# Kernel optimization log

Measured on AMD Instinct MI355X. Metric: run time of the kernel, lower is better.

Reference implementation:

```python
import jax, jax.numpy as jnp
import numpy as np

B, L, E = 2, 2048, 1024
H = 16
DH = E // H  # head dim for qk and v (dim_qk=dim_v=embed_dim)
HID = 4 * E  # fcn_dim_factor * dim_v
SCALE = DH ** 0.5


def setup_inputs() -> dict:
    key = jax.random.key(0)
    ks = jax.random.split(key, 12)
    s = lambda fan_in: 1.0 / np.sqrt(fan_in)
    return {
        "x": jax.random.uniform(ks[0], (B, L), jnp.float32),
        "z": jax.random.normal(ks[1], (B, L, E), jnp.float32),
        "Wq": jax.random.normal(ks[2], (E, E), jnp.float32) * s(E),
        "bq": jnp.zeros((E,), jnp.float32),
        "Wk": jax.random.normal(ks[3], (E, E), jnp.float32) * s(E),
        "bk": jnp.zeros((E,), jnp.float32),
        "Wv": jax.random.normal(ks[4], (E, E), jnp.float32) * s(E),
        "bv": jnp.zeros((E,), jnp.float32),
        "W1": jax.random.normal(ks[5], (E, HID), jnp.float32) * s(E),
        "b1": jnp.zeros((HID,), jnp.float32),
        "W2": jax.random.normal(ks[6], (HID, 1), jnp.float32) * s(HID),
        "b2": jnp.zeros((1,), jnp.float32),
    }


def reference(x, z, Wq, bq, Wk, bk, Wv, bv, W1, b1, W2, b2):
    # Projections -> (B, H, L, DH)
    def heads(t):
        return t.reshape(B, L, H, DH).transpose(0, 2, 1, 3)

    Q = heads(z @ Wq + bq)
    K = heads(z @ Wk + bk)
    V = heads(z @ Wv + bv)

    # Scores (B, H, L, L)
    S = jnp.einsum("bhid,bhjd->bhij", Q, K) / SCALE

    # Weighted softmax along query axis (dim=-2), weighted by population x
    w = x[:, None, :, None]  # (B, 1, L, 1), broadcasts over queries i
    m = jnp.max(S, axis=-2, keepdims=True)
    e = w * jnp.exp(S - m)
    A = e / jnp.sum(e, axis=-2, keepdims=True)

    # V scaled by population weight, then AV
    V_scaled = w * V
    O = jnp.einsum("bhij,bhjd->bhid", A, V_scaled)  # (B, H, L, DH)
    O = O.transpose(0, 2, 1, 3).reshape(B, L, H * DH)

    # FFN: Linear -> GELU (exact) -> Linear(->1) -> squeeze
    y = jax.nn.gelu(O @ W1 + b1, approximate=False)
    y = (y @ W2 + b2).squeeze(-1)  # (B, L)
    return y
```

## Files before the change

### kernel.cpp

```cpp
#include <hip/hip_runtime.h>
#include <hip/hip_bf16.h>
#include <math.h>

#define B_    2
#define L_    2048
#define E_    1024
#define H_    16
#define DH_   64
#define HID_  4096
#define NROW_ (B_*L_)
#define BH_   (B_*H_)

typedef __attribute__((ext_vector_type(8)))  short    short8v;
typedef _Float16 half8v __attribute__((ext_vector_type(8)));
typedef __attribute__((ext_vector_type(16))) float    f32x16;

#define MFMA32(A, Bv, C) __builtin_amdgcn_mfma_f32_32x32x16_bf16((A), (Bv), (C), 0, 0, 0)
#define MFMAH(A, Bv, C)  __builtin_amdgcn_mfma_f32_32x32x16_f16((A), (Bv), (C), 0, 0, 0)

__device__ __forceinline__ unsigned short f2bf(float f) {
    union { float f; unsigned u; } v; v.f = f;
    unsigned r = v.u + 0x7FFF + ((v.u >> 16) & 1);
    return (unsigned short)(r >> 16);
}
__device__ __forceinline__ float bf2f(unsigned short u) {
    union { unsigned u; float f; } v; v.u = ((unsigned)u) << 16;
    return v.f;
}

__device__ __forceinline__ void gl_lds16(const void* g, void* l) {
    __builtin_amdgcn_global_load_lds(
        (const __attribute__((address_space(1))) unsigned int*)g,
        (__attribute__((address_space(3))) unsigned int*)l, 16, 0, 0);
}

__device__ __forceinline__ float erf_fast(float v) {
    float a = fabsf(v);
    float t = __builtin_amdgcn_rcpf(1.0f + 0.3275911f * a);
    float p = t * (0.254829592f + t * (-0.284496736f + t * (1.421413741f +
              t * (-1.453152027f + t * 1.061405429f))));
    float r = 1.0f - p * __expf(-a * a);
    return copysignf(r, v);
}

__global__ __launch_bounds__(256) void zh_prep(
    const float* __restrict__ z, _Float16* __restrict__ zh)
{
    const size_t i = ((size_t)blockIdx.x * 256 + threadIdx.x) * 8;
    float4 a = *(const float4*)&z[i];
    float4 b = *(const float4*)&z[i + 4];
    union { _Float16 h[8]; half8v v; } o;
    o.h[0] = (_Float16)a.x; o.h[1] = (_Float16)a.y;
    o.h[2] = (_Float16)a.z; o.h[3] = (_Float16)a.w;
    o.h[4] = (_Float16)b.x; o.h[5] = (_Float16)b.y;
    o.h[6] = (_Float16)b.z; o.h[7] = (_Float16)b.w;
    *(half8v*)&zh[i] = o.v;
}

__global__ __launch_bounds__(256) void wprep3(
    const float* __restrict__ Wq, const float* __restrict__ Wk,
    const float* __restrict__ Wv,
    _Float16* __restrict__ Tq, _Float16* __restrict__ Tk,
    _Float16* __restrict__ Tv)
{
    const float* src = (blockIdx.z == 0) ? Wq : (blockIdx.z == 1) ? Wk : Wv;
    _Float16*    dst = (blockIdx.z == 0) ? Tq : (blockIdx.z == 1) ? Tk : Tv;
    __shared__ float tile[64][65];
    const int t  = threadIdx.x;
    const int r0 = blockIdx.y * 64, c0 = blockIdx.x * 64;
    #pragma unroll
    for (int u = 0; u < 4; ++u) {
        int f = t + 256 * u, row = f >> 4, c4 = (f & 15) << 2;
        *(float4*)&tile[row][c4] = *(const float4*)&src[(size_t)(r0 + row) * E_ + c0 + c4];
    }
    __syncthreads();
    #pragma unroll
    for (int u = 0; u < 4; ++u) {
        int f = t + 256 * u, c = f >> 4, r4 = (f & 15) << 2;
        union { _Float16 h[4]; uint2 u2; } pk;
        pk.h[0] = (_Float16)tile[r4 + 0][c];
        pk.h[1] = (_Float16)tile[r4 + 1][c];
        pk.h[2] = (_Float16)tile[r4 + 2][c];
        pk.h[3] = (_Float16)tile[r4 + 3][c];
        *(uint2*)&dst[(size_t)(c0 + c) * E_ + r0 + r4] = pk.u2;
    }
}

__global__ __launch_bounds__(256) void w1prep(
    const float* __restrict__ W1, _Float16* __restrict__ W1t)
{
    __shared__ float tile[64][65];
    const int t  = threadIdx.x;
    const int r0 = blockIdx.y * 64, c0 = blockIdx.x * 64;
    #pragma unroll
    for (int u = 0; u < 4; ++u) {
        int f = t + 256 * u, row = f >> 4, c4 = (f & 15) << 2;
        *(float4*)&tile[row][c4] = *(const float4*)&W1[(size_t)(r0 + row) * HID_ + c0 + c4];
    }
    __syncthreads();
    #pragma unroll
    for (int u = 0; u < 4; ++u) {
        int f = t + 256 * u, c = f >> 4, r4 = (f & 15) << 2;
        union { _Float16 h[4]; uint2 u2; } pk;
        pk.h[0] = (_Float16)tile[r4 + 0][c];
        pk.h[1] = (_Float16)tile[r4 + 1][c];
        pk.h[2] = (_Float16)tile[r4 + 2][c];
        pk.h[3] = (_Float16)tile[r4 + 3][c];
        *(uint2*)&W1t[(size_t)(c0 + c) * E_ + r0 + r4] = pk.u2;
    }
}

__global__ __launch_bounds__(512) void qkv_mfma(
    const _Float16* __restrict__ zh,
    const _Float16* __restrict__ Tq, const _Float16* __restrict__ Tk,
    const _Float16* __restrict__ Tv,
    const float* __restrict__ bq, const float* __restrict__ bk,
    const float* __restrict__ bv,
    unsigned short* __restrict__ Qo, unsigned short* __restrict__ Ko,
    unsigned short* __restrict__ Vo)
{
    const int which = blockIdx.z;
    const _Float16* Wt = (which == 0) ? Tq : (which == 1) ? Tk : Tv;
    const float*  bias = (which == 0) ? bq : (which == 1) ? bk : bv;
    unsigned short* out = (which == 0) ? Qo : (which == 1) ? Ko : Vo;

    __shared__ _Float16 Ah[256 * 64];
    __shared__ _Float16 Bs[256 * 64];

    const int t    = threadIdx.x;
    const int lane = t & 63;
    const int w    = t >> 6;
    const int l31  = lane & 31;
    const int hq   = lane >> 5;
    const int wm   = w >> 2, wn = w & 3;
    const int m0   = blockIdx.x * 256;
    const int n0   = blockIdx.y * 256;

    f32x16 acc[4][2] = {};

    for (int kc = 0; kc < 16; ++kc) {
        __syncthreads();
        #pragma unroll
        for (int u = 0; u < 4; ++u) {
            int ch  = w * 4 + u;
            int row = ch * 8 + (lane >> 3), s = lane & 7;
            gl_lds16(&zh[(size_t)(m0 + row) * E_ + kc * 64 + ((s ^ (row & 7)) << 3)], &Ah[ch * 512]);
            gl_lds16(&Wt[(size_t)(n0 + row) * E_ + kc * 64 + ((s ^ (row & 7)) << 3)], &Bs[ch * 512]);
        }
        __syncthreads();

        #pragma unroll
        for (int ks = 0; ks < 4; ++ks) {
            half8v fb[2];
            #pragma unroll
            for (int nb = 0; nb < 2; ++nb) {
                int br = wn * 64 + nb * 32 + l31;
                fb[nb] = *(const half8v*)&Bs[br * 64 + (((ks * 2 + hq) ^ (br & 7)) << 3)];
            }
            #pragma unroll
            for (int mb = 0; mb < 4; ++mb) {
                int ar = wm * 128 + mb * 32 + l31;
                half8v fa = *(const half8v*)&Ah[ar * 64 + (((ks * 2 + hq) ^ (ar & 7)) << 3)];
                acc[mb][0] = MFMAH(fa, fb[0], acc[mb][0]);
                acc[mb][1] = MFMAH(fa, fb[1], acc[mb][1]);
            }
        }
    }

    #pragma unroll
    for (int nb = 0; nb < 2; ++nb) {
        int n  = n0 + wn * 64 + nb * 32 + l31;
        int h  = n >> 6, dh = n & 63;
        float bb = bias[n];
        #pragma unroll
        for (int mb = 0; mb < 4; ++mb) {
            #pragma unroll
            for (int r = 0; r < 16; ++r) {
                int m  = m0 + wm * 128 + mb * 32 + (r & 3) + 8 * (r >> 2) + 4 * hq;
                int b  = m >> 11, i = m & (L_ - 1);
                out[((size_t)(b * H_ + h) * L_ + i) * DH_ + dh] = f2bf(acc[mb][nb][r] + bb);
            }
        }
    }
}

__global__ __launch_bounds__(256) void col_stats_mfma(
    const unsigned short* __restrict__ Qb, const unsigned short* __restrict__ Kb,
    const float* __restrict__ x, float* __restrict__ Do)
{
    __shared__ unsigned short Qlds[128 * 64];
    __shared__ float xlds[L_];

    const int t    = threadIdx.x;
    const int lane = t & 63;
    const int wv   = t >> 6;
    const int l31  = lane & 31;
    const int hq   = lane >> 5;
    const int bh   = blockIdx.y;
    const int b    = bh >> 4;
    const int j0   = blockIdx.x * 128 + wv * 32;

    #pragma unroll
    for (int u = 0; u < 2; ++u) {
        int f = t + 256 * u;
        *(float4*)&xlds[f * 4] = *(const float4*)&x[(size_t)b * L_ + f * 4];
    }

    short8v kf[4];
    {
        const unsigned short* kp = Kb + ((size_t)bh * L_ + j0 + l31) * DH_ + hq * 8;
        #pragma unroll
        for (int c = 0; c < 4; ++c) kf[c] = *(const short8v*)(kp + c * 16);
    }

    float d[16];
    #pragma unroll
    for (int r = 0; r < 16; ++r) d[r] = 0.f;

    for (int ich = 0; ich < L_ / 128; ++ich) {
        __syncthreads();
        #pragma unroll
        for (int u = 0; u < 4; ++u) {
            int ch  = wv * 4 + u;
            int row = ch * 8 + (lane >> 3), s = lane & 7;
            gl_lds16(&Qb[((size_t)bh * L_ + ich * 128 + row) * DH_ + ((s ^ (row & 7)) << 3)],
                     &Qlds[ch * 512]);
        }
        __syncthreads();

        #pragma unroll
        for (int cc = 0; cc < 4; ++cc) {
            f32x16 acc = {};
            #pragma unroll
            for (int c = 0; c < 4; ++c) {
                int qr = cc * 32 + l31;
                short8v qv = *(const short8v*)&Qlds[qr * 64 + (((c * 2 + hq) ^ (qr & 7)) << 3)];
                acc = MFMA32(kf[c], qv, acc);
            }
            float xi = xlds[ich * 128 + cc * 32 + l31];
            #pragma unroll
            for (int r = 0; r < 16; ++r)
                d[r] += xi * __expf(acc[r] * 0.125f);
        }
    }

    #pragma unroll
    for (int r = 0; r < 16; ++r) {
        #pragma unroll
        for (int off = 16; off > 0; off >>= 1)
            d[r] += __shfl_xor(d[r], off);
    }
    if (l31 == 0) {
        #pragma unroll
        for (int r = 0; r < 16; ++r)
            Do[(size_t)bh * L_ + j0 + 4 * hq + (r & 3) + 8 * (r >> 2)] = d[r];
    }
}

__global__ __launch_bounds__(256) void vt_prep(
    const unsigned short* __restrict__ Vb, const float* __restrict__ x,
    const float* __restrict__ Do, unsigned short* __restrict__ Vt)
{
    const int bh = blockIdx.y;
    const int b  = bh >> 4;
    const int j  = blockIdx.x * 256 + threadIdx.x;
    const float s = x[(size_t)b * L_ + j] / Do[(size_t)bh * L_ + j];
    const unsigned short* vp = Vb + ((size_t)bh * L_ + j) * DH_;
    #pragma unroll
    for (int c = 0; c < 16; ++c) {
        ushort4 v = *(const ushort4*)&vp[c * 4];
        Vt[((size_t)bh * DH_ + c * 4 + 0) * L_ + j] = f2bf(bf2f(v.x) * s);
        Vt[((size_t)bh * DH_ + c * 4 + 1) * L_ + j] = f2bf(bf2f(v.y) * s);
        Vt[((size_t)bh * DH_ + c * 4 + 2) * L_ + j] = f2bf(bf2f(v.z) * s);
        Vt[((size_t)bh * DH_ + c * 4 + 3) * L_ + j] = f2bf(bf2f(v.w) * s);
    }
}

__global__ __launch_bounds__(256) void attn_out_mfma(
    const unsigned short* __restrict__ Qb, const unsigned short* __restrict__ Kb,
    const unsigned short* __restrict__ Vt, const float* __restrict__ x,
    _Float16* __restrict__ Of)
{
    __shared__ unsigned short Klds[64 * 64];
    __shared__ unsigned short Vlds[64 * 64];
    __shared__ unsigned short Plds[4 * 32 * 64];

    const int t    = threadIdx.x;
    const int lane = t & 63;
    const int wv   = t >> 6;
    const int l31  = lane & 31;
    const int hq   = lane >> 5;
    const int bh   = blockIdx.y;
    const int b    = bh >> 4, hh = bh & 15;
    const int iw   = blockIdx.x * 128 + wv * 32;

    short8v qf[4];
    {
        const unsigned short* qp = Qb + ((size_t)bh * L_ + iw + l31) * DH_ + hq * 8;
        #pragma unroll
        for (int c = 0; c < 4; ++c) qf[c] = *(const short8v*)(qp + c * 16);
    }

    f32x16 accO0 = {}, accO1 = {};
    char* Pw = (char*)(Plds + wv * 2048);

    for (int jt = 0; jt < L_ / 64; ++jt) {
        int j0 = jt * 64;
        __syncthreads();
        #pragma unroll
        for (int u = 0; u < 2; ++u) {
            int ch  = wv * 2 + u;
            int row = ch * 8 + (lane >> 3), s = lane & 7;
            gl_lds16(&Kb[((size_t)bh * L_ + j0 + row) * DH_ + ((s ^ (row & 7)) << 3)], &Klds[ch * 512]);
            gl_lds16(&Vt[((size_t)bh * DH_ + row) * L_ + j0 + ((s ^ (row & 7)) << 3)], &Vlds[ch * 512]);
        }
        __syncthreads();

        #pragma unroll
        for (int js = 0; js < 2; ++js) {
            f32x16 as = {};
            #pragma unroll
            for (int c = 0; c < 4; ++c) {
                int krow = js * 32 + l31;
                short8v kfr = *(const short8v*)&Klds[krow * 64 + (((c * 2 + hq) ^ (krow & 7)) << 3)];
                as = MFMA32(kfr, qf[c], as);
            }
            #pragma unroll
            for (int q = 0; q < 4; ++q) {
                float p0 = __expf(as[4 * q + 0] * 0.125f);
                float p1 = __expf(as[4 * q + 1] * 0.125f);
                float p2 = __expf(as[4 * q + 2] * 0.125f);
                float p3 = __expf(as[4 * q + 3] * 0.125f);
                uint2 pk;
                pk.x = (unsigned)f2bf(p0) | ((unsigned)f2bf(p1) << 16);
                pk.y = (unsigned)f2bf(p2) | ((unsigned)f2bf(p3) << 16);
                int jb = js * 64 + 8 * hq + 16 * q;
                *(uint2*)(Pw + l31 * 128 + (jb ^ ((l31 & 7) << 4))) = pk;
            }
        }

        short8v pf[4];
        #pragma unroll
        for (int c = 0; c < 4; ++c)
            pf[c] = *(const short8v*)(Pw + l31 * 128 + (((c * 16 + hq * 8) * 2) ^ ((l31 & 7) << 4)));
        #pragma unroll
        for (int c = 0; c < 4; ++c) {
            int r0 = l31, r1 = 32 + l31;
            short8v vf0 = *(const short8v*)&Vlds[r0 * 64 + (((c * 2 + hq) ^ (r0 & 7)) << 3)];
            short8v vf1 = *(const short8v*)&Vlds[r1 * 64 + (((c * 2 + hq) ^ (r1 & 7)) << 3)];
            accO0 = MFMA32(pf[c], vf0, accO0);
            accO1 = MFMA32(pf[c], vf1, accO1);
        }
    }

    #pragma unroll
    for (int q = 0; q < 4; ++q) {
        float4 xq = *(const float4*)&x[(size_t)b * L_ + iw + 4 * hq + 8 * q];
        const float xs[4] = { xq.x, xq.y, xq.z, xq.w };
        #pragma unroll
        for (int k = 0; k < 4; ++k) {
            int r    = q * 4 + k;
            int irow = iw + 4 * hq + 8 * q + k;
            size_t base = ((size_t)b * L_ + irow) * E_ + hh * DH_;
            Of[base + l31]      = (_Float16)(accO0[r] * xs[k]);
            Of[base + 32 + l31] = (_Float16)(accO1[r] * xs[k]);
        }
    }
}

__global__ __launch_bounds__(256) void y_init(float* __restrict__ y, const float* __restrict__ b2)
{
    y[blockIdx.x * 256 + threadIdx.x] = b2[0];
}

__global__ __launch_bounds__(512) void mlp_mfma(
    const _Float16* __restrict__ Of, const _Float16* __restrict__ W1t,
    const float* __restrict__ b1, const float* __restrict__ W2,
    float* __restrict__ y)
{
    __shared__ _Float16 Oh[256 * 64];
    __shared__ _Float16 Wh[256 * 64];

    const int t    = threadIdx.x;
    const int lane = t & 63;
    const int w    = t >> 6;
    const int l31  = lane & 31;
    const int hq   = lane >> 5;
    const int wm   = w >> 2, wn = w & 3;
    const int m0   = blockIdx.x * 256;
    const int n0   = blockIdx.y * 256;

    f32x16 acc[4][2] = {};

    for (int kc = 0; kc < 16; ++kc) {
        __syncthreads();
        #pragma unroll
        for (int u = 0; u < 4; ++u) {
            int ch  = w * 4 + u;
            int row = ch * 8 + (lane >> 3), s = lane & 7;
            gl_lds16(&Of[(size_t)(m0 + row) * E_ + kc * 64 + ((s ^ (row & 7)) << 3)], &Oh[ch * 512]);
            gl_lds16(&W1t[(size_t)(n0 + row) * E_ + kc * 64 + ((s ^ (row & 7)) << 3)], &Wh[ch * 512]);
        }
        __syncthreads();

        #pragma unroll
        for (int ks = 0; ks < 4; ++ks) {
            half8v fb[2];
            #pragma unroll
            for (int nb = 0; nb < 2; ++nb) {
                int br = wn * 64 + nb * 32 + l31;
                fb[nb] = *(const half8v*)&Wh[br * 64 + (((ks * 2 + hq) ^ (br & 7)) << 3)];
            }
            #pragma unroll
            for (int mb = 0; mb < 4; ++mb) {
                int ar = wm * 128 + mb * 32 + l31;
                half8v fa = *(const half8v*)&Oh[ar * 64 + (((ks * 2 + hq) ^ (ar & 7)) << 3)];
                acc[mb][0] = MFMAH(fa, fb[0], acc[mb][0]);
                acc[mb][1] = MFMAH(fa, fb[1], acc[mb][1]);
            }
        }
    }

    const int hid0 = n0 + wn * 64 + l31;
    const float bb0 = b1[hid0],      w20 = W2[hid0];
    const float bb1 = b1[hid0 + 32], w21 = W2[hid0 + 32];
    #pragma unroll
    for (int mb = 0; mb < 4; ++mb) {
        #pragma unroll
        for (int r = 0; r < 16; ++r) {
            float h0 = acc[mb][0][r] + bb0;
            float h1 = acc[mb][1][r] + bb1;
            float s  = 0.5f * h0 * (1.0f + erf_fast(h0 * 0.70710678f)) * w20
                     + 0.5f * h1 * (1.0f + erf_fast(h1 * 0.70710678f)) * w21;
            #pragma unroll
            for (int off = 16; off > 0; off >>= 1) s += __shfl_xor(s, off);
            if (l31 == 0) {
                int m = m0 + wm * 128 + mb * 32 + (r & 3) + 8 * (r >> 2) + 4 * hq;
                atomicAdd(&y[m], s);
            }
        }
    }
}

extern "C" void kernel_launch(void* const* d_in, const int* in_sizes, int n_in,
                              void* d_out, int out_size, void* d_ws, size_t ws_size,
                              hipStream_t stream)
{
    const float* x  = (const float*)d_in[0];
    const float* z  = (const float*)d_in[1];
    const float* Wq = (const float*)d_in[2];
    const float* bq = (const float*)d_in[3];
    const float* Wk = (const float*)d_in[4];
    const float* bk = (const float*)d_in[5];
    const float* Wv = (const float*)d_in[6];
    const float* bv = (const float*)d_in[7];
    const float* W1 = (const float*)d_in[8];
    const float* b1 = (const float*)d_in[9];
    const float* W2 = (const float*)d_in[10];
    const float* b2 = (const float*)d_in[11];
    float* y = (float*)d_out;

    const size_t NQ = (size_t)BH_ * L_ * DH_;
    unsigned short* p = (unsigned short*)d_ws;
    unsigned short* Qb  = p;  p += NQ;
    unsigned short* Kb  = p;  p += NQ;
    unsigned short* Vb  = p;  p += NQ;
    unsigned short* Vt  = p;  p += NQ;
    _Float16* zh  = (_Float16*)p;  p += (size_t)NROW_ * E_;
    _Float16* Tq  = (_Float16*)p;  p += (size_t)E_ * E_;
    _Float16* Tk  = (_Float16*)p;  p += (size_t)E_ * E_;
    _Float16* Tv  = (_Float16*)p;  p += (size_t)E_ * E_;
    _Float16* W1t = (_Float16*)p;  p += (size_t)HID_ * E_;
    _Float16* Ofp = (_Float16*)p;  p += (size_t)NROW_ * E_;
    float* Dw = (float*)p;

    zh_prep<<<dim3((NROW_ * E_) / (256 * 8)), 256, 0, stream>>>(z, zh);
    wprep3 <<<dim3(E_ / 64, E_ / 64, 3), 256, 0, stream>>>(Wq, Wk, Wv, Tq, Tk, Tv);
    w1prep <<<dim3(HID_ / 64, E_ / 64), 256, 0, stream>>>(W1, W1t);

    qkv_mfma<<<dim3(NROW_ / 256, E_ / 256, 3), 512, 0, stream>>>(
        zh, Tq, Tk, Tv, bq, bk, bv, Qb, Kb, Vb);

    col_stats_mfma<<<dim3(L_ / 128, BH_), 256, 0, stream>>>(Qb, Kb, x, Dw);

    vt_prep<<<dim3(L_ / 256, BH_), 256, 0, stream>>>(Vb, x, Dw, Vt);

    attn_out_mfma<<<dim3(L_ / 128, BH_), 256, 0, stream>>>(Qb, Kb, Vt, x, Ofp);

    y_init<<<dim3(NROW_ / 256), 256, 0, stream>>>(y, b2);

    mlp_mfma<<<dim3(NROW_ / 256, HID_ / 256), 512, 0, stream>>>(
        Ofp, W1t, b1, W2, y);
}
```

Baseline: 231.8 us.

## Double-buffer LDS tiles in GEMM and attention kernels to overlap loads with MFMA

Adds ping-pong LDS buffers to qkv_mfma, col_stats_mfma, attn_out_mfma and mlp_mfma. The next k-chunk is issued with global-to-LDS loads before the current chunk's MFMAs run, and each iteration ends with one barrier. The goal is to hide global load latency behind compute. In exchange, LDS use doubles: the GEMM kernels go to 128KB per block, which can cut occupancy to one block per CU. It also depends on the async LDS loads being complete by the time the single barrier is reached.

```diff
diff --git a/kernel.cpp b/kernel.cpp
--- a/kernel.cpp
+++ b/kernel.cpp
@@ -124,8 +124,8 @@
     const float*  bias = (which == 0) ? bq : (which == 1) ? bk : bv;
     unsigned short* out = (which == 0) ? Qo : (which == 1) ? Ko : Vo;
 
-    __shared__ _Float16 Ah[256 * 64];
-    __shared__ _Float16 Bs[256 * 64];
+    __shared__ _Float16 Ah[2][256 * 64];
+    __shared__ _Float16 Bs[2][256 * 64];
 
     const int t    = threadIdx.x;
     const int lane = t & 63;
@@ -136,18 +136,30 @@
     const int m0   = blockIdx.x * 256;
     const int n0   = blockIdx.y * 256;
 
+    const int srow0 = (lane >> 3);
+    const int ssl   = lane & 7;
+
     f32x16 acc[4][2] = {};
 
+#define QKV_STAGE(bb, kc)                                                          \
+    {                                                                              \
+        _Pragma("unroll")                                                          \
+        for (int u = 0; u < 4; ++u) {                                              \
+            int ch  = w * 4 + u;                                                   \
+            int row = ch * 8 + srow0;                                              \
+            gl_lds16(&zh[(size_t)(m0 + row) * E_ + (kc) * 64 + ((ssl ^ (row & 7)) << 3)], \
+                     &Ah[bb][ch * 512]);                                           \
+            gl_lds16(&Wt[(size_t)(n0 + row) * E_ + (kc) * 64 + ((ssl ^ (row & 7)) << 3)], \
+                     &Bs[bb][ch * 512]);                                           \
+        }                                                                          \
+    }
+
+    QKV_STAGE(0, 0);
+    __syncthreads();
+    int cur = 0;
+
     for (int kc = 0; kc < 16; ++kc) {
-        __syncthreads();
-        #pragma unroll
-        for (int u = 0; u < 4; ++u) {
-            int ch  = w * 4 + u;
-            int row = ch * 8 + (lane >> 3), s = lane & 7;
-            gl_lds16(&zh[(size_t)(m0 + row) * E_ + kc * 64 + ((s ^ (row & 7)) << 3)], &Ah[ch * 512]);
-            gl_lds16(&Wt[(size_t)(n0 + row) * E_ + kc * 64 + ((s ^ (row & 7)) << 3)], &Bs[ch * 512]);
-        }
-        __syncthreads();
+        if (kc < 15) QKV_STAGE(cur ^ 1, kc + 1);
 
         #pragma unroll
         for (int ks = 0; ks < 4; ++ks) {
@@ -155,16 +167,18 @@
             #pragma unroll
             for (int nb = 0; nb < 2; ++nb) {
                 int br = wn * 64 + nb * 32 + l31;
-                fb[nb] = *(const half8v*)&Bs[br * 64 + (((ks * 2 + hq) ^ (br & 7)) << 3)];
+                fb[nb] = *(const half8v*)&Bs[cur][br * 64 + (((ks * 2 + hq) ^ (br & 7)) << 3)];
             }
             #pragma unroll
             for (int mb = 0; mb < 4; ++mb) {
                 int ar = wm * 128 + mb * 32 + l31;
-                half8v fa = *(const half8v*)&Ah[ar * 64 + (((ks * 2 + hq) ^ (ar & 7)) << 3)];
+                half8v fa = *(const half8v*)&Ah[cur][ar * 64 + (((ks * 2 + hq) ^ (ar & 7)) << 3)];
                 acc[mb][0] = MFMAH(fa, fb[0], acc[mb][0]);
                 acc[mb][1] = MFMAH(fa, fb[1], acc[mb][1]);
             }
         }
+        __syncthreads();
+        cur ^= 1;
     }
 
     #pragma unroll
@@ -182,13 +196,14 @@
             }
         }
     }
+#undef QKV_STAGE
 }
 
 __global__ __launch_bounds__(256) void col_stats_mfma(
     const unsigned short* __restrict__ Qb, const unsigned short* __restrict__ Kb,
     const float* __restrict__ x, float* __restrict__ Do)
 {
-    __shared__ unsigned short Qlds[128 * 64];
+    __shared__ unsigned short Qlds[2][128 * 64];
     __shared__ float xlds[L_];
 
     const int t    = threadIdx.x;
@@ -200,6 +215,9 @@
     const int b    = bh >> 4;
     const int j0   = blockIdx.x * 128 + wv * 32;
 
+    const int srow0 = (lane >> 3);
+    const int ssl   = lane & 7;
+
     #pragma unroll
     for (int u = 0; u < 2; ++u) {
         int f = t + 256 * u;
@@ -217,16 +235,23 @@
     #pragma unroll
     for (int r = 0; r < 16; ++r) d[r] = 0.f;
 
+#define CS_STAGE(bb, ich)                                                           \
+    {                                                                               \
+        _Pragma("unroll")                                                           \
+        for (int u = 0; u < 4; ++u) {                                               \
+            int ch  = wv * 4 + u;                                                   \
+            int row = ch * 8 + srow0;                                               \
+            gl_lds16(&Qb[((size_t)bh * L_ + (ich) * 128 + row) * DH_ + ((ssl ^ (row & 7)) << 3)], \
+                     &Qlds[bb][ch * 512]);                                          \
+        }                                                                           \
+    }
+
+    CS_STAGE(0, 0);
+    __syncthreads();
+    int cur = 0;
+
     for (int ich = 0; ich < L_ / 128; ++ich) {
-        __syncthreads();
-        #pragma unroll
-        for (int u = 0; u < 4; ++u) {
-            int ch  = wv * 4 + u;
-            int row = ch * 8 + (lane >> 3), s = lane & 7;
-            gl_lds16(&Qb[((size_t)bh * L_ + ich * 128 + row) * DH_ + ((s ^ (row & 7)) << 3)],
-                     &Qlds[ch * 512]);
-        }
-        __syncthreads();
+        if (ich < L_ / 128 - 1) CS_STAGE(cur ^ 1, ich + 1);
 
         #pragma unroll
         for (int cc = 0; cc < 4; ++cc) {
@@ -234,7 +259,7 @@
             #pragma unroll
             for (int c = 0; c < 4; ++c) {
                 int qr = cc * 32 + l31;
-                short8v qv = *(const short8v*)&Qlds[qr * 64 + (((c * 2 + hq) ^ (qr & 7)) << 3)];
+                short8v qv = *(const short8v*)&Qlds[cur][qr * 64 + (((c * 2 + hq) ^ (qr & 7)) << 3)];
                 acc = MFMA32(kf[c], qv, acc);
             }
             float xi = xlds[ich * 128 + cc * 32 + l31];
@@ -242,6 +267,8 @@
             for (int r = 0; r < 16; ++r)
                 d[r] += xi * __expf(acc[r] * 0.125f);
         }
+        __syncthreads();
+        cur ^= 1;
     }
 
     #pragma unroll
@@ -255,6 +282,7 @@
         for (int r = 0; r < 16; ++r)
             Do[(size_t)bh * L_ + j0 + 4 * hq + (r & 3) + 8 * (r >> 2)] = d[r];
     }
+#undef CS_STAGE
 }
 
 __global__ __launch_bounds__(256) void vt_prep(
@@ -281,8 +309,8 @@
     const unsigned short* __restrict__ Vt, const float* __restrict__ x,
     _Float16* __restrict__ Of)
 {
-    __shared__ unsigned short Klds[64 * 64];
-    __shared__ unsigned short Vlds[64 * 64];
+    __shared__ unsigned short Klds[2][64 * 64];
+    __shared__ unsigned short Vlds[2][64 * 64];
     __shared__ unsigned short Plds[4 * 32 * 64];
 
     const int t    = threadIdx.x;
@@ -294,6 +322,9 @@
     const int b    = bh >> 4, hh = bh & 15;
     const int iw   = blockIdx.x * 128 + wv * 32;
 
+    const int srow0 = (lane >> 3);
+    const int ssl   = lane & 7;
+
     short8v qf[4];
     {
         const unsigned short* qp = Qb + ((size_t)bh * L_ + iw + l31) * DH_ + hq * 8;
@@ -304,17 +335,25 @@
     f32x16 accO0 = {}, accO1 = {};
     char* Pw = (char*)(Plds + wv * 2048);
 
+#define AO_STAGE(bb, jt)                                                            \
+    {                                                                               \
+        _Pragma("unroll")                                                           \
+        for (int u = 0; u < 2; ++u) {                                               \
+            int ch  = wv * 2 + u;                                                   \
+            int row = ch * 8 + srow0;                                               \
+            gl_lds16(&Kb[((size_t)bh * L_ + (jt) * 64 + row) * DH_ + ((ssl ^ (row & 7)) << 3)], \
+                     &Klds[bb][ch * 512]);                                          \
+            gl_lds16(&Vt[((size_t)bh * DH_ + row) * L_ + (jt) * 64 + ((ssl ^ (row & 7)) << 3)], \
+                     &Vlds[bb][ch * 512]);                                          \
+        }                                                                           \
+    }
+
+    AO_STAGE(0, 0);
+    __syncthreads();
+    int cur = 0;
+
     for (int jt = 0; jt < L_ / 64; ++jt) {
-        int j0 = jt * 64;
-        __syncthreads();
-        #pragma unroll
-        for (int u = 0; u < 2; ++u) {
-            int ch  = wv * 2 + u;
-            int row = ch * 8 + (lane >> 3), s = lane & 7;
-            gl_lds16(&Kb[((size_t)bh * L_ + j0 + row) * DH_ + ((s ^ (row & 7)) << 3)], &Klds[ch * 512]);
-            gl_lds16(&Vt[((size_t)bh * DH_ + row) * L_ + j0 + ((s ^ (row & 7)) << 3)], &Vlds[ch * 512]);
-        }
-        __syncthreads();
+        if (jt < L_ / 64 - 1) AO_STAGE(cur ^ 1, jt + 1);
 
         #pragma unroll
         for (int js = 0; js < 2; ++js) {
@@ -322,7 +361,7 @@
             #pragma unroll
             for (int c = 0; c < 4; ++c) {
                 int krow = js * 32 + l31;
-                short8v kfr = *(const short8v*)&Klds[krow * 64 + (((c * 2 + hq) ^ (krow & 7)) << 3)];
+                short8v kfr = *(const short8v*)&Klds[cur][krow * 64 + (((c * 2 + hq) ^ (krow & 7)) << 3)];
                 as = MFMA32(kfr, qf[c], as);
             }
             #pragma unroll
@@ -346,11 +385,13 @@
         #pragma unroll
         for (int c = 0; c < 4; ++c) {
             int r0 = l31, r1 = 32 + l31;
-            short8v vf0 = *(const short8v*)&Vlds[r0 * 64 + (((c * 2 + hq) ^ (r0 & 7)) << 3)];
-            short8v vf1 = *(const short8v*)&Vlds[r1 * 64 + (((c * 2 + hq) ^ (r1 & 7)) << 3)];
+            short8v vf0 = *(const short8v*)&Vlds[cur][r0 * 64 + (((c * 2 + hq) ^ (r0 & 7)) << 3)];
+            short8v vf1 = *(const short8v*)&Vlds[cur][r1 * 64 + (((c * 2 + hq) ^ (r1 & 7)) << 3)];
             accO0 = MFMA32(pf[c], vf0, accO0);
             accO1 = MFMA32(pf[c], vf1, accO1);
         }
+        __syncthreads();
+        cur ^= 1;
     }
 
     #pragma unroll
@@ -366,6 +407,7 @@
             Of[base + 32 + l31] = (_Float16)(accO1[r] * xs[k]);
         }
     }
+#undef AO_STAGE
 }
 
 __global__ __launch_bounds__(256) void y_init(float* __restrict__ y, const float* __restrict__ b2)
@@ -378,8 +420,8 @@
     const float* __restrict__ b1, const float* __restrict__ W2,
     float* __restrict__ y)
 {
-    __shared__ _Float16 Oh[256 * 64];
-    __shared__ _Float16 Wh[256 * 64];
+    __shared__ _Float16 Oh[2][256 * 64];
+    __shared__ _Float16 Wh[2][256 * 64];
 
     const int t    = threadIdx.x;
     const int lane = t & 63;
@@ -390,18 +432,30 @@
     const int m0   = blockIdx.x * 256;
     const int n0   = blockIdx.y * 256;
 
+    const int srow0 = (lane >> 3);
+    const int ssl   = lane & 7;
+
     f32x16 acc[4][2] = {};
 
+#define MLP_STAGE(bb, kc)                                                          \
+    {                                                                              \
+        _Pragma("unroll")                                                          \
+        for (int u = 0; u < 4; ++u) {                                              \
+            int ch  = w * 4 + u;                                                   \
+            int row = ch * 8 + srow0;                                              \
+            gl_lds16(&Of[(size_t)(m0 + row) * E_ + (kc) * 64 + ((ssl ^ (row & 7)) << 3)], \
+                     &Oh[bb][ch * 512]);                                           \
+            gl_lds16(&W1t[(size_t)(n0 + row) * E_ + (kc) * 64 + ((ssl ^ (row & 7)) << 3)], \
+                     &Wh[bb][ch * 512]);                                           \
+        }                                                                          \
+    }
+
+    MLP_STAGE(0, 0);
+    __syncthreads();
+    int cur = 0;
+
     for (int kc = 0; kc < 16; ++kc) {
-        __syncthreads();
-        #pragma unroll
-        for (int u = 0; u < 4; ++u) {
-            int ch  = w * 4 + u;
-            int row = ch * 8 + (lane >> 3), s = lane & 7;
-            gl_lds16(&Of[(size_t)(m0 + row) * E_ + kc * 64 + ((s ^ (row & 7)) << 3)], &Oh[ch * 512]);
-            gl_lds16(&W1t[(size_t)(n0 + row) * E_ + kc * 64 + ((s ^ (row & 7)) << 3)], &Wh[ch * 512]);
-        }
-        __syncthreads();
+        if (kc < 15) MLP_STAGE(cur ^ 1, kc + 1);
 
         #pragma unroll
         for (int ks = 0; ks < 4; ++ks) {
@@ -409,16 +463,18 @@
             #pragma unroll
             for (int nb = 0; nb < 2; ++nb) {
                 int br = wn * 64 + nb * 32 + l31;
-                fb[nb] = *(const half8v*)&Wh[br * 64 + (((ks * 2 + hq) ^ (br & 7)) << 3)];
+                fb[nb] = *(const half8v*)&Wh[cur][br * 64 + (((ks * 2 + hq) ^ (br & 7)) << 3)];
             }
             #pragma unroll
             for (int mb = 0; mb < 4; ++mb) {
                 int ar = wm * 128 + mb * 32 + l31;
-                half8v fa = *(const half8v*)&Oh[ar * 64 + (((ks * 2 + hq) ^ (ar & 7)) << 3)];
+                half8v fa = *(const half8v*)&Oh[cur][ar * 64 + (((ks * 2 + hq) ^ (ar & 7)) << 3)];
                 acc[mb][0] = MFMAH(fa, fb[0], acc[mb][0]);
                 acc[mb][1] = MFMAH(fa, fb[1], acc[mb][1]);
             }
         }
+        __syncthreads();
+        cur ^= 1;
     }
 
     const int hid0 = n0 + wn * 64 + l31;
@@ -440,6 +496,7 @@
             }
         }
     }
+#undef MLP_STAGE
 }
 
 extern "C" void kernel_launch(void* const* d_in, const int* in_sizes, int n_in,
```

Measured after the change: 237.7 us. 2.5% more time.
